# Kernel optimization log

Hardware: AMD Instinct MI355X
Metric: run time of the kernel (lower is better)

## Reference

```python
import jax, jax.numpy as jnp
import numpy as np

N_EMBED = 1024
HEAD_SIZE = 128
B, T = 4, 4096

def setup_inputs() -> dict:
    key = jax.random.key(0)
    kx, kk, kq, kv = jax.random.split(key, 4)
    s = (1.0 / np.sqrt(N_EMBED)).astype(np.float32)
    return {
        "x": jax.random.normal(kx, (B, T, N_EMBED), dtype=jnp.float32),
        "W_key": jax.random.normal(kk, (N_EMBED, HEAD_SIZE), dtype=jnp.float32) * s,
        "W_query": jax.random.normal(kq, (N_EMBED, HEAD_SIZE), dtype=jnp.float32) * s,
        "W_value": jax.random.normal(kv, (N_EMBED, HEAD_SIZE), dtype=jnp.float32) * s,
    }

def reference(x, W_key, W_query, W_value):
    # x: [B,T,C]; single-head causal attention. NOTE: scale is C**-0.5 (n_embed),
    # matching the original source (not head_size**-0.5).
    Bn, Tn, C = x.shape
    k = jnp.einsum('btc,cd->btd', x, W_key)    # [B,T,d]
    q = jnp.einsum('btc,cd->btd', x, W_query)  # [B,T,d]
    v = jnp.einsum('btc,cd->btd', x, W_value)  # [B,T,d]
    scores = jnp.einsum('btd,bsd->bts', q, k) * (C ** -0.5)  # [B,T,T]
    causal = jnp.tril(jnp.ones((Tn, Tn), dtype=bool))
    scores = jnp.where(causal[None, :, :], scores, -jnp.inf)
    attn = jax.nn.softmax(scores, axis=-1)
    return jnp.einsum('bts,bsd->btd', attn, v)
```

## Files before the change

### kernel.cpp

```cpp
#include <hip/hip_runtime.h>
#include <hip/hip_bf16.h>

typedef __attribute__((ext_vector_type(8))) short bf16x8;
typedef __attribute__((ext_vector_type(4))) float f32x4;
typedef __attribute__((ext_vector_type(4))) unsigned short us4;

__device__ __forceinline__ unsigned short f2bf(float f) {
    union { float f; unsigned u; } c; c.f = f;
    unsigned u = c.u;
    u += 0x7fffu + ((u >> 16) & 1u);
    return (unsigned short)(u >> 16);
}
__device__ __forceinline__ float bf2f(unsigned short h) {
    union { unsigned u; float f; } c; c.u = ((unsigned)h) << 16;
    return c.f;
}
__device__ __forceinline__ unsigned cvt_pk_bf16(float lo, float hi) {
    unsigned r;
    asm volatile("v_cvt_pk_bf16_f32 %0, %1, %2" : "=v"(r) : "v"(lo), "v"(hi));
    return r;
}
__device__ __forceinline__ void gload_lds16(const void* g, void* l) {
    __builtin_amdgcn_global_load_lds(
        (const __attribute__((address_space(1))) unsigned int*)g,
        (__attribute__((address_space(3))) unsigned int*)l, 16, 0, 0);
}

#define QSCALE 0.04508422f

__global__ __launch_bounds__(256) void wconv_kernel(
        const float* __restrict__ Wk, const float* __restrict__ Wq,
        const float* __restrict__ Wv, unsigned short* __restrict__ WbT) {
    int idx = blockIdx.x * 256 + threadIdx.x;
    int n = idx >> 10, kk = idx & 1023;
    const float* W = (n < 128) ? Wk : (n < 256) ? Wq : Wv;
    int col = n & 127;
    WbT[idx] = f2bf(W[kk * 128 + col]);
}

__global__ __launch_bounds__(512) void qkv_gemm_kernel(
        const float* __restrict__ x, const unsigned short* __restrict__ WbT,
        unsigned short* __restrict__ kw, unsigned short* __restrict__ qw,
        unsigned short* __restrict__ vTw) {
    __shared__ __align__(16) unsigned short Bl[2][192 * 64];
    __shared__ __align__(16) unsigned short Al[2][64 * 72];
    const int tid = threadIdx.x;
    const int m0 = (blockIdx.x >> 1) * 64;
    const int nb = blockIdx.x & 1;
    const int w = tid >> 6, l = tid & 63;
    const int l15 = l & 15, lh = l >> 4;
    const int wm = w >> 2, wn = w & 3;

    f32x4 acc[2][3] = {};

    const int srcsw = ((((l & 7) * 16) ^ ((l >> 3) << 4)) >> 1);
    const unsigned short* gB[3];
    #pragma unroll
    for (int it = 0; it < 3; ++it)
        gB[it] = WbT + (size_t)(nb * 192 + it * 64 + w * 8 + (l >> 3)) * 1024 + srcsw;

    const float* xr = &x[(size_t)(m0 + (tid >> 3)) * 1024 + (tid & 7) * 8];
    const int aoff = (tid >> 3) * 72 + (tid & 7) * 8;

    float4 aE0, aE1, aO0, aO1;

    #define STAGE_B(buf, t_) do { \
        _Pragma("unroll") \
        for (int it = 0; it < 3; ++it) \
            gload_lds16(gB[it] + (t_) * 64, &Bl[buf][(it * 64 + w * 8) * 64]); \
    } while (0)
    #define ISSUE_A(d0, d1, t_) do { \
        d0 = *(const float4*)(xr + (t_) * 64); \
        d1 = *(const float4*)(xr + (t_) * 64 + 4); } while (0)
    #define WRITE_A(buf, s0, s1) do { \
        uint4 pk_; \
        pk_.x = cvt_pk_bf16(s0.x, s0.y); pk_.y = cvt_pk_bf16(s0.z, s0.w); \
        pk_.z = cvt_pk_bf16(s1.x, s1.y); pk_.w = cvt_pk_bf16(s1.z, s1.w); \
        *(uint4*)&Al[buf][aoff] = pk_; } while (0)
    #define MFMA_ON(buf) do { \
        for (int kc = 0; kc < 2; ++kc) { \
            bf16x8 a_[2], bb_[3]; \
            for (int mi = 0; mi < 2; ++mi) \
                a_[mi] = *(const bf16x8*)&Al[buf][(wm * 32 + mi * 16 + l15) * 72 + kc * 32 + lh * 8]; \
            for (int ni = 0; ni < 3; ++ni) { \
                int n_ = wn * 48 + ni * 16 + l15; \
                bb_[ni] = *(const bf16x8*)((const char*)Bl[buf] + n_ * 128 + \
                        ((kc * 64 + lh * 16) ^ ((n_ & 7) << 4))); \
            } \
            for (int mi = 0; mi < 2; ++mi) \
                for (int ni = 0; ni < 3; ++ni) \
                    acc[mi][ni] = __builtin_amdgcn_mfma_f32_16x16x32_bf16( \
                            a_[mi], bb_[ni], acc[mi][ni], 0, 0, 0); \
        } } while (0)
    #define BAR(n_) do { \
        asm volatile("s_waitcnt vmcnt(" #n_ ") lgkmcnt(0)" ::: "memory"); \
        __builtin_amdgcn_sched_barrier(0); \
        __builtin_amdgcn_s_barrier(); } while (0)

    STAGE_B(0, 0);
    ISSUE_A(aE0, aE1, 0);
    ISSUE_A(aO0, aO1, 1);
    WRITE_A(0, aE0, aE1);
    BAR(2);

    #pragma unroll 1
    for (int tt = 0; tt < 8; ++tt) {
        const int t0 = tt * 2;
        STAGE_B(1, t0 + 1);
        if (t0 + 2 < 16) ISSUE_A(aE0, aE1, t0 + 2);
        MFMA_ON(0);
        WRITE_A(1, aO0, aO1);
        if (t0 + 2 < 16) BAR(2); else BAR(0);
        if (t0 + 2 < 16) {
            STAGE_B(0, t0 + 2);
            if (t0 + 3 < 16) ISSUE_A(aO0, aO1, t0 + 3);
            MFMA_ON(1);
            WRITE_A(0, aE0, aE1);
            if (t0 + 3 < 16) BAR(2); else BAR(0);
        } else {
            MFMA_ON(1);
        }
    }
    #undef STAGE_B
    #undef ISSUE_A
    #undef WRITE_A
    #undef MFMA_ON
    #undef BAR

    for (int mi = 0; mi < 2; ++mi)
        for (int ni = 0; ni < 3; ++ni) {
            int col = nb * 192 + wn * 48 + ni * 16 + l15;
            int sect = col >> 7, cc = col & 127;
            if (sect < 2) {
                unsigned short* dst = (sect == 0) ? kw : qw;
                float fs = (sect == 0) ? 1.0f : QSCALE;
                for (int i = 0; i < 4; ++i) {
                    int row = m0 + wm * 32 + mi * 16 + lh * 4 + i;
                    dst[(size_t)row * 128 + cc] = f2bf(acc[mi][ni][i] * fs);
                }
            } else {
                int trow0 = m0 + wm * 32 + mi * 16 + lh * 4;
                int b = trow0 >> 12, t0_ = trow0 & 4095;
                union { unsigned short u[4]; us4 v; } pk;
                for (int i = 0; i < 4; ++i) pk.u[i] = f2bf(acc[mi][ni][i]);
                *(us4*)&vTw[((size_t)(b * 128 + cc)) * 4096 + t0_] = pk.v;
            }
        }
}

__global__ __launch_bounds__(512) void attn_kernel(
        const unsigned short* __restrict__ kw, const unsigned short* __restrict__ qw,
        const unsigned short* __restrict__ vTw,
        unsigned short* __restrict__ pO, float* __restrict__ pL,
        int nCPB, int G, int TPC) {
    __shared__ __align__(16) unsigned short Kl[2][64 * 128];
    __shared__ __align__(16) unsigned short Vl[2][128 * 64];
    __shared__ __align__(16) unsigned short Pl[8][1024];

    const int tid = threadIdx.x;
    const int wgid = blockIdx.x;
    const int xcd = wgid & 7, slot = wgid >> 3;
    const int b = xcd >> 1, half = xcd & 1;
    const int cid = (nCPB - 1) - (slot * 2 + half);
    const int halfG = G >> 1;
    int a = 0;
    while (halfG * (a + 1) * (a + 2) <= cid) ++a;
    int rem = cid - halfG * a * (a + 1);
    const int g = G * a + rem / (a + 1);
    const int c = rem % (a + 1);
    const int kt0 = c * TPC;
    const int kt1 = min(kt0 + TPC, 2 * g + 2);

    const int w = tid >> 6, l = tid & 63;
    const int l15 = l & 15, lh = l >> 4;
    const int qrow0 = g * 128 + w * 16;

    bf16x8 qa[4];
    {
        size_t grow = (size_t)b * 4096 + qrow0 + l15;
        for (int cc = 0; cc < 4; ++cc)
            qa[cc] = *(const bf16x8*)&qw[grow * 128 + cc * 32 + lh * 8];
    }
    bf16x8 ones;
    for (int u = 0; u < 8; ++u) ones[u] = (short)0x3F80;

    f32x4 o[8] = {};
    f32x4 lsa = {0.f, 0.f, 0.f, 0.f};

    const int kc0 = 2 * w, kc1 = 2 * w + 1;
    const int kr0 = 4 * kc0 + (l >> 4), kr1 = 4 * kc1 + (l >> 4);
    const unsigned short* gk0 = kw + ((size_t)(b * 4096 + kr0)) * 128 +
            (((((l & 15) * 16) ^ ((kr0 & 7) << 4))) >> 1);
    const unsigned short* gk1 = kw + ((size_t)(b * 4096 + kr1)) * 128 +
            (((((l & 15) * 16) ^ ((kr1 & 7) << 4))) >> 1);
    const int vd0 = 8 * kc0 + (l >> 3), vd1 = 8 * kc1 + (l >> 3);
    const unsigned short* gv0 = vTw + ((size_t)(b * 128 + vd0)) * 4096 +
            (((((l & 7) * 16) ^ ((vd0 & 7) << 4))) >> 1);
    const unsigned short* gv1 = vTw + ((size_t)(b * 128 + vd1)) * 4096 +
            (((((l & 7) * 16) ^ ((vd1 & 7) << 4))) >> 1);

    #define STAGE(B_, kt_) do { \
        int kv_ = (kt_) * 64; \
        gload_lds16(gk0 + (size_t)kv_ * 128, &Kl[B_][kc0 * 512]); \
        gload_lds16(gk1 + (size_t)kv_ * 128, &Kl[B_][kc1 * 512]); \
        gload_lds16(gv0 + kv_, &Vl[B_][kc0 * 512]); \
        gload_lds16(gv1 + kv_, &Vl[B_][kc1 * 512]); } while (0)

    char* Plw = (char*)&Pl[w][0];

    STAGE(0, kt0);
    __syncthreads();
    int cur = 0;
    for (int kt = kt0; kt < kt1; ++kt) {
        if (kt + 1 < kt1) STAGE(cur ^ 1, kt + 1);
        const int kv0 = kt * 64;
        if (kv0 <= qrow0 + 15) {
            const char* Kc = (const char*)Kl[cur];
            const char* Vc = (const char*)Vl[cur];
            f32x4 s[4];
            __builtin_amdgcn_s_setprio(1);
            for (int ni = 0; ni < 4; ++ni) {
                s[ni] = (f32x4){0.f, 0.f, 0.f, 0.f};
                int kr = ni * 16 + l15;
                int sw = (kr & 7) << 4;
                for (int cc = 0; cc < 4; ++cc) {
                    bf16x8 bk = *(bf16x8*)(Kc + kr * 256 + ((lh * 16 + cc * 64) ^ sw));
                    s[ni] = __builtin_amdgcn_mfma_f32_16x16x32_bf16(bk, qa[cc], s[ni], 0, 0, 0);
                }
            }
            __builtin_amdgcn_s_setprio(0);

            if (kv0 + 63 > qrow0) {
                int qg = qrow0 + l15;
                for (int ni = 0; ni < 4; ++ni)
                    for (int i = 0; i < 4; ++i)
                        if (kv0 + ni * 16 + lh * 4 + i > qg) s[ni][i] = -INFINITY;
            }
            for (int ni = 0; ni < 4; ++ni) {
                float p0 = exp2f(s[ni][0]), p1 = exp2f(s[ni][1]);
                float p2 = exp2f(s[ni][2]), p3 = exp2f(s[ni][3]);
                uint2 pk;
                pk.x = cvt_pk_bf16(p0, p1);
                pk.y = cvt_pk_bf16(p2, p3);
                *(uint2*)(Plw + l15 * 128 + ((ni * 32 + lh * 8) ^ ((l15 & 7) << 4))) = pk;
            }
            bf16x8 pa[2];
            for (int kc = 0; kc < 2; ++kc)
                pa[kc] = *(bf16x8*)(Plw + l15 * 128 +
                        ((kc * 64 + lh * 16) ^ ((l15 & 7) << 4)));
            __builtin_amdgcn_s_setprio(1);
            lsa = __builtin_amdgcn_mfma_f32_16x16x32_bf16(pa[1], ones,
                  __builtin_amdgcn_mfma_f32_16x16x32_bf16(pa[0], ones, lsa, 0, 0, 0), 0, 0, 0);
            for (int nd = 0; nd < 8; ++nd) {
                int dr = nd * 16 + l15;
                int sw = (dr & 7) << 4;
                for (int kc = 0; kc < 2; ++kc) {
                    bf16x8 bv = *(bf16x8*)(Vc + dr * 128 + ((lh * 16 + kc * 64) ^ sw));
                    o[nd] = __builtin_amdgcn_mfma_f32_16x16x32_bf16(pa[kc], bv, o[nd], 0, 0, 0);
                }
            }
            __builtin_amdgcn_s_setprio(0);
        }
        __syncthreads();
        cur ^= 1;
    }
    #undef STAGE

    const int slot_ = b * nCPB + cid;
    unsigned short* po = pO + (size_t)slot_ * 16384;
    for (int nd = 0; nd < 8; ++nd)
        for (int i = 0; i < 4; ++i)
            po[(w * 16 + lh * 4 + i) * 128 + nd * 16 + l15] = f2bf(o[nd][i]);
    if (l15 == 0) {
        float* pl = pL + (size_t)slot_ * 128;
        for (int i = 0; i < 4; ++i)
            pl[w * 16 + lh * 4 + i] = lsa[i];
    }
}

__global__ __launch_bounds__(256) void combine_kernel(
        const unsigned short* __restrict__ pO, const float* __restrict__ pL,
        float* __restrict__ out, int nCPB, int G) {
    int idx = blockIdx.x * 256 + threadIdx.x;
    int row = idx >> 4, d8 = (idx & 15) * 8;
    int b = row >> 12, t = row & 4095;
    int g = t >> 7, rowin = t & 127;
    int a = g / G;
    int nch = a + 1;
    int base = b * nCPB + (G >> 1) * a * (a + 1) + (g - G * a) * (a + 1);

    float den = 0.f;
    float num[8] = {0.f, 0.f, 0.f, 0.f, 0.f, 0.f, 0.f, 0.f};
    for (int cc = 0; cc < nch; ++cc) {
        den += pL[(size_t)(base + cc) * 128 + rowin];
        bf16x8 ov = *(const bf16x8*)&pO[(size_t)(base + cc) * 16384 + rowin * 128 + d8];
        for (int u = 0; u < 8; ++u)
            num[u] += bf2f((unsigned short)ov[u]);
    }
    float inv = 1.f / den;
    for (int u = 0; u < 8; ++u)
        out[(size_t)row * 128 + d8 + u] = num[u] * inv;
}

extern "C" void kernel_launch(void* const* d_in, const int* in_sizes, int n_in,
                              void* d_out, int out_size, void* d_ws, size_t ws_size,
                              hipStream_t stream) {
    const float* x  = (const float*)d_in[0];
    const float* Wk = (const float*)d_in[1];
    const float* Wq = (const float*)d_in[2];
    const float* Wv = (const float*)d_in[3];
    float* out = (float*)d_out;

    char* ws = (char*)d_ws;
    unsigned short* WbT = (unsigned short*)(ws);
    unsigned short* kw  = (unsigned short*)(ws + 786432);
    unsigned short* qw  = (unsigned short*)(ws + 786432 + 4194304);
    unsigned short* vTw = (unsigned short*)(ws + 786432 + 2 * 4194304);
    size_t base = 786432 + 3 * (size_t)4194304;

    int nCPB, G, TPC;
    size_t need4 = base + (size_t)1088 * 32768 + (size_t)1088 * 512;
    if (ws_size >= need4) { nCPB = 272; G = 2; TPC = 4; }
    else                  { nCPB = 144; G = 4; TPC = 8; }
    int nslots = 4 * nCPB;
    unsigned short* pO = (unsigned short*)(ws + base);
    float*          pL = (float*)(ws + base + (size_t)nslots * 32768);

    wconv_kernel<<<1536, 256, 0, stream>>>(Wk, Wq, Wv, WbT);
    qkv_gemm_kernel<<<512, 512, 0, stream>>>(x, WbT, kw, qw, vTw);
    attn_kernel<<<nslots, 512, 0, stream>>>(kw, qw, vTw, pO, pL, nCPB, G, TPC);
    combine_kernel<<<1024, 256, 0, stream>>>(pO, pL, out, nCPB, G);
}
```

Before: 81.79 us.

## Double query rows per warp and stage K/V through registers

Each warp now handles 32 query rows (two 16-row MFMA tiles) instead of 16, so every K and V fragment read from LDS feeds twice as many MFMAs. The work split becomes fixed 256-row query groups with 4-tile KV chunks, giving 544 workgroups and half the partial slots for the combine step. The async global-to-LDS double buffer is replaced by a register prefetch with a single LDS buffer and two barriers per tile. This raises register pressure and drops the workspace-size fallback path.

```diff
diff --git a/kernel.cpp b/kernel.cpp
--- a/kernel.cpp
+++ b/kernel.cpp
@@ -151,149 +151,158 @@
 __global__ __launch_bounds__(512) void attn_kernel(
         const unsigned short* __restrict__ kw, const unsigned short* __restrict__ qw,
         const unsigned short* __restrict__ vTw,
-        unsigned short* __restrict__ pO, float* __restrict__ pL,
-        int nCPB, int G, int TPC) {
-    __shared__ __align__(16) unsigned short Kl[2][64 * 128];
-    __shared__ __align__(16) unsigned short Vl[2][128 * 64];
-    __shared__ __align__(16) unsigned short Pl[8][1024];
+        unsigned short* __restrict__ pO, float* __restrict__ pL) {
+    __shared__ __align__(16) unsigned short Kl[64 * 128];
+    __shared__ __align__(16) unsigned short Vl[128 * 64];
+    __shared__ __align__(16) unsigned short Pl[8][2048];
 
     const int tid = threadIdx.x;
     const int wgid = blockIdx.x;
     const int xcd = wgid & 7, slot = wgid >> 3;
-    const int b = xcd >> 1, half = xcd & 1;
-    const int cid = (nCPB - 1) - (slot * 2 + half);
-    const int halfG = G >> 1;
-    int a = 0;
-    while (halfG * (a + 1) * (a + 2) <= cid) ++a;
-    int rem = cid - halfG * a * (a + 1);
-    const int g = G * a + rem / (a + 1);
-    const int c = rem % (a + 1);
-    const int kt0 = c * TPC;
-    const int kt1 = min(kt0 + TPC, 2 * g + 2);
+    const int b = xcd >> 1;
+    const int cid = (xcd & 1) * 68 + slot;
+    int g = 0;
+    while ((g + 1) * (g + 2) / 2 <= cid) ++g;
+    const int c = cid - g * (g + 1) / 2;
+    const int kt0 = c * 4, kt1 = kt0 + 4;
 
     const int w = tid >> 6, l = tid & 63;
     const int l15 = l & 15, lh = l >> 4;
-    const int qrow0 = g * 128 + w * 16;
-
-    bf16x8 qa[4];
+    const int qrow0 = g * 256 + w * 32;
+
+    bf16x8 qa0[4], qa1[4];
     {
-        size_t grow = (size_t)b * 4096 + qrow0 + l15;
-        for (int cc = 0; cc < 4; ++cc)
-            qa[cc] = *(const bf16x8*)&qw[grow * 128 + cc * 32 + lh * 8];
+        size_t gr0 = (size_t)b * 4096 + qrow0 + l15;
+        size_t gr1 = gr0 + 16;
+        for (int cc = 0; cc < 4; ++cc) {
+            qa0[cc] = *(const bf16x8*)&qw[gr0 * 128 + cc * 32 + lh * 8];
+            qa1[cc] = *(const bf16x8*)&qw[gr1 * 128 + cc * 32 + lh * 8];
+        }
     }
     bf16x8 ones;
     for (int u = 0; u < 8; ++u) ones[u] = (short)0x3F80;
 
-    f32x4 o[8] = {};
-    f32x4 lsa = {0.f, 0.f, 0.f, 0.f};
-
-    const int kc0 = 2 * w, kc1 = 2 * w + 1;
-    const int kr0 = 4 * kc0 + (l >> 4), kr1 = 4 * kc1 + (l >> 4);
-    const unsigned short* gk0 = kw + ((size_t)(b * 4096 + kr0)) * 128 +
-            (((((l & 15) * 16) ^ ((kr0 & 7) << 4))) >> 1);
-    const unsigned short* gk1 = kw + ((size_t)(b * 4096 + kr1)) * 128 +
-            (((((l & 15) * 16) ^ ((kr1 & 7) << 4))) >> 1);
-    const int vd0 = 8 * kc0 + (l >> 3), vd1 = 8 * kc1 + (l >> 3);
-    const unsigned short* gv0 = vTw + ((size_t)(b * 128 + vd0)) * 4096 +
-            (((((l & 7) * 16) ^ ((vd0 & 7) << 4))) >> 1);
-    const unsigned short* gv1 = vTw + ((size_t)(b * 128 + vd1)) * 4096 +
-            (((((l & 7) * 16) ^ ((vd1 & 7) << 4))) >> 1);
-
-    #define STAGE(B_, kt_) do { \
-        int kv_ = (kt_) * 64; \
-        gload_lds16(gk0 + (size_t)kv_ * 128, &Kl[B_][kc0 * 512]); \
-        gload_lds16(gk1 + (size_t)kv_ * 128, &Kl[B_][kc1 * 512]); \
-        gload_lds16(gv0 + kv_, &Vl[B_][kc0 * 512]); \
-        gload_lds16(gv1 + kv_, &Vl[B_][kc1 * 512]); } while (0)
+    f32x4 o0[8] = {}, o1[8] = {};
+    f32x4 lsa0 = {0.f, 0.f, 0.f, 0.f}, lsa1 = {0.f, 0.f, 0.f, 0.f};
+
+    const int kr_ = tid >> 3;
+    const int vd_ = tid >> 2;
+    bf16x8 kReg[2], vReg[2];
+    auto issue = [&](int kt) {
+        int kv0 = kt * 64;
+        const unsigned short* ks = &kw[((size_t)(b * 4096 + kv0 + kr_)) * 128 + (tid & 7) * 16];
+        kReg[0] = *(const bf16x8*)ks;
+        kReg[1] = *(const bf16x8*)(ks + 8);
+        const unsigned short* vs = &vTw[((size_t)(b * 128 + vd_)) * 4096 + kv0 + (tid & 3) * 16];
+        vReg[0] = *(const bf16x8*)vs;
+        vReg[1] = *(const bf16x8*)(vs + 8);
+    };
 
     char* Plw = (char*)&Pl[w][0];
 
-    STAGE(0, kt0);
-    __syncthreads();
-    int cur = 0;
+    issue(kt0);
     for (int kt = kt0; kt < kt1; ++kt) {
-        if (kt + 1 < kt1) STAGE(cur ^ 1, kt + 1);
+        __syncthreads();
+        for (int it = 0; it < 2; ++it)
+            *(bf16x8*)((char*)Kl + kr_ * 256 +
+                    (((tid & 7) * 32 + it * 16) ^ ((kr_ & 7) << 4))) = kReg[it];
+        for (int it = 0; it < 2; ++it)
+            *(bf16x8*)((char*)Vl + vd_ * 128 +
+                    (((tid & 3) * 32 + it * 16) ^ ((vd_ & 7) << 4))) = vReg[it];
+        __syncthreads();
+        if (kt + 1 < kt1) issue(kt + 1);
+
         const int kv0 = kt * 64;
-        if (kv0 <= qrow0 + 15) {
-            const char* Kc = (const char*)Kl[cur];
-            const char* Vc = (const char*)Vl[cur];
-            f32x4 s[4];
-            __builtin_amdgcn_s_setprio(1);
-            for (int ni = 0; ni < 4; ++ni) {
-                s[ni] = (f32x4){0.f, 0.f, 0.f, 0.f};
-                int kr = ni * 16 + l15;
-                int sw = (kr & 7) << 4;
-                for (int cc = 0; cc < 4; ++cc) {
-                    bf16x8 bk = *(bf16x8*)(Kc + kr * 256 + ((lh * 16 + cc * 64) ^ sw));
-                    s[ni] = __builtin_amdgcn_mfma_f32_16x16x32_bf16(bk, qa[cc], s[ni], 0, 0, 0);
+        if (kv0 > qrow0 + 31) continue;
+
+        f32x4 s0[4], s1[4];
+        __builtin_amdgcn_s_setprio(1);
+        for (int ni = 0; ni < 4; ++ni) {
+            s0[ni] = (f32x4){0.f, 0.f, 0.f, 0.f};
+            s1[ni] = (f32x4){0.f, 0.f, 0.f, 0.f};
+            int kr = ni * 16 + l15;
+            int sw = (kr & 7) << 4;
+            for (int cc = 0; cc < 4; ++cc) {
+                bf16x8 bk = *(bf16x8*)((char*)Kl + kr * 256 + ((lh * 16 + cc * 64) ^ sw));
+                s0[ni] = __builtin_amdgcn_mfma_f32_16x16x32_bf16(bk, qa0[cc], s0[ni], 0, 0, 0);
+                s1[ni] = __builtin_amdgcn_mfma_f32_16x16x32_bf16(bk, qa1[cc], s1[ni], 0, 0, 0);
+            }
+        }
+        __builtin_amdgcn_s_setprio(0);
+
+        if (kv0 + 63 > qrow0) {
+            int q0 = qrow0 + l15, q1 = q0 + 16;
+            for (int ni = 0; ni < 4; ++ni)
+                for (int i = 0; i < 4; ++i) {
+                    int kvp = kv0 + ni * 16 + lh * 4 + i;
+                    if (kvp > q0) s0[ni][i] = -INFINITY;
+                    if (kvp > q1) s1[ni][i] = -INFINITY;
                 }
+        }
+        for (int ni = 0; ni < 4; ++ni) {
+            uint2 pk;
+            pk.x = cvt_pk_bf16(exp2f(s0[ni][0]), exp2f(s0[ni][1]));
+            pk.y = cvt_pk_bf16(exp2f(s0[ni][2]), exp2f(s0[ni][3]));
+            *(uint2*)(Plw + l15 * 128 + ((ni * 32 + lh * 8) ^ ((l15 & 7) << 4))) = pk;
+            pk.x = cvt_pk_bf16(exp2f(s1[ni][0]), exp2f(s1[ni][1]));
+            pk.y = cvt_pk_bf16(exp2f(s1[ni][2]), exp2f(s1[ni][3]));
+            *(uint2*)(Plw + (16 + l15) * 128 + ((ni * 32 + lh * 8) ^ ((l15 & 7) << 4))) = pk;
+        }
+        bf16x8 pa0[2], pa1[2];
+        for (int kc = 0; kc < 2; ++kc) {
+            pa0[kc] = *(bf16x8*)(Plw + l15 * 128 +
+                    ((kc * 64 + lh * 16) ^ ((l15 & 7) << 4)));
+            pa1[kc] = *(bf16x8*)(Plw + (16 + l15) * 128 +
+                    ((kc * 64 + lh * 16) ^ ((l15 & 7) << 4)));
+        }
+        __builtin_amdgcn_s_setprio(1);
+        lsa0 = __builtin_amdgcn_mfma_f32_16x16x32_bf16(pa0[1], ones,
+               __builtin_amdgcn_mfma_f32_16x16x32_bf16(pa0[0], ones, lsa0, 0, 0, 0), 0, 0, 0);
+        lsa1 = __builtin_amdgcn_mfma_f32_16x16x32_bf16(pa1[1], ones,
+               __builtin_amdgcn_mfma_f32_16x16x32_bf16(pa1[0], ones, lsa1, 0, 0, 0), 0, 0, 0);
+        for (int nd = 0; nd < 8; ++nd) {
+            int dr = nd * 16 + l15;
+            int sw = (dr & 7) << 4;
+            for (int kc = 0; kc < 2; ++kc) {
+                bf16x8 bv = *(bf16x8*)((char*)Vl + dr * 128 + ((lh * 16 + kc * 64) ^ sw));
+                o0[nd] = __builtin_amdgcn_mfma_f32_16x16x32_bf16(pa0[kc], bv, o0[nd], 0, 0, 0);
+                o1[nd] = __builtin_amdgcn_mfma_f32_16x16x32_bf16(pa1[kc], bv, o1[nd], 0, 0, 0);
             }
-            __builtin_amdgcn_s_setprio(0);
-
-            if (kv0 + 63 > qrow0) {
-                int qg = qrow0 + l15;
-                for (int ni = 0; ni < 4; ++ni)
-                    for (int i = 0; i < 4; ++i)
-                        if (kv0 + ni * 16 + lh * 4 + i > qg) s[ni][i] = -INFINITY;
-            }
-            for (int ni = 0; ni < 4; ++ni) {
-                float p0 = exp2f(s[ni][0]), p1 = exp2f(s[ni][1]);
-                float p2 = exp2f(s[ni][2]), p3 = exp2f(s[ni][3]);
-                uint2 pk;
-                pk.x = cvt_pk_bf16(p0, p1);
-                pk.y = cvt_pk_bf16(p2, p3);
-                *(uint2*)(Plw + l15 * 128 + ((ni * 32 + lh * 8) ^ ((l15 & 7) << 4))) = pk;
-            }
-            bf16x8 pa[2];
-            for (int kc = 0; kc < 2; ++kc)
-                pa[kc] = *(bf16x8*)(Plw + l15 * 128 +
-                        ((kc * 64 + lh * 16) ^ ((l15 & 7) << 4)));
-            __builtin_amdgcn_s_setprio(1);
-            lsa = __builtin_amdgcn_mfma_f32_16x16x32_bf16(pa[1], ones,
-                  __builtin_amdgcn_mfma_f32_16x16x32_bf16(pa[0], ones, lsa, 0, 0, 0), 0, 0, 0);
-            for (int nd = 0; nd < 8; ++nd) {
-                int dr = nd * 16 + l15;
-                int sw = (dr & 7) << 4;
-                for (int kc = 0; kc < 2; ++kc) {
-                    bf16x8 bv = *(bf16x8*)(Vc + dr * 128 + ((lh * 16 + kc * 64) ^ sw));
-                    o[nd] = __builtin_amdgcn_mfma_f32_16x16x32_bf16(pa[kc], bv, o[nd], 0, 0, 0);
-                }
-            }
-            __builtin_amdgcn_s_setprio(0);
-        }
-        __syncthreads();
-        cur ^= 1;
-    }
-    #undef STAGE
-
-    const int slot_ = b * nCPB + cid;
-    unsigned short* po = pO + (size_t)slot_ * 16384;
+        }
+        __builtin_amdgcn_s_setprio(0);
+    }
+
+    const int slot_ = b * 136 + cid;
+    unsigned short* po = pO + (size_t)slot_ * 32768;
     for (int nd = 0; nd < 8; ++nd)
-        for (int i = 0; i < 4; ++i)
-            po[(w * 16 + lh * 4 + i) * 128 + nd * 16 + l15] = f2bf(o[nd][i]);
+        for (int i = 0; i < 4; ++i) {
+            po[(w * 32 + lh * 4 + i) * 128 + nd * 16 + l15]      = f2bf(o0[nd][i]);
+            po[(w * 32 + 16 + lh * 4 + i) * 128 + nd * 16 + l15] = f2bf(o1[nd][i]);
+        }
     if (l15 == 0) {
-        float* pl = pL + (size_t)slot_ * 128;
-        for (int i = 0; i < 4; ++i)
-            pl[w * 16 + lh * 4 + i] = lsa[i];
+        float* pl = pL + (size_t)slot_ * 256;
+        for (int i = 0; i < 4; ++i) {
+            pl[w * 32 + lh * 4 + i]      = lsa0[i];
+            pl[w * 32 + 16 + lh * 4 + i] = lsa1[i];
+        }
     }
 }
 
 __global__ __launch_bounds__(256) void combine_kernel(
         const unsigned short* __restrict__ pO, const float* __restrict__ pL,
-        float* __restrict__ out, int nCPB, int G) {
+        float* __restrict__ out) {
     int idx = blockIdx.x * 256 + threadIdx.x;
     int row = idx >> 4, d8 = (idx & 15) * 8;
     int b = row >> 12, t = row & 4095;
-    int g = t >> 7, rowin = t & 127;
-    int a = g / G;
-    int nch = a + 1;
-    int base = b * nCPB + (G >> 1) * a * (a + 1) + (g - G * a) * (a + 1);
+    int g = t >> 8, rowin = t & 255;
+    int nch = g + 1;
+    int base = b * 136 + g * (g + 1) / 2;
 
     float den = 0.f;
     float num[8] = {0.f, 0.f, 0.f, 0.f, 0.f, 0.f, 0.f, 0.f};
     for (int cc = 0; cc < nch; ++cc) {
-        den += pL[(size_t)(base + cc) * 128 + rowin];
-        bf16x8 ov = *(const bf16x8*)&pO[(size_t)(base + cc) * 16384 + rowin * 128 + d8];
+        den += pL[(size_t)(base + cc) * 256 + rowin];
+        bf16x8 ov = *(const bf16x8*)&pO[(size_t)(base + cc) * 32768 + rowin * 128 + d8];
         for (int u = 0; u < 8; ++u)
             num[u] += bf2f((unsigned short)ov[u]);
     }
@@ -317,17 +326,11 @@
     unsigned short* qw  = (unsigned short*)(ws + 786432 + 4194304);
     unsigned short* vTw = (unsigned short*)(ws + 786432 + 2 * 4194304);
     size_t base = 786432 + 3 * (size_t)4194304;
-
-    int nCPB, G, TPC;
-    size_t need4 = base + (size_t)1088 * 32768 + (size_t)1088 * 512;
-    if (ws_size >= need4) { nCPB = 272; G = 2; TPC = 4; }
-    else                  { nCPB = 144; G = 4; TPC = 8; }
-    int nslots = 4 * nCPB;
     unsigned short* pO = (unsigned short*)(ws + base);
-    float*          pL = (float*)(ws + base + (size_t)nslots * 32768);
+    float*          pL = (float*)(ws + base + (size_t)544 * 65536);
 
     wconv_kernel<<<1536, 256, 0, stream>>>(Wk, Wq, Wv, WbT);
     qkv_gemm_kernel<<<512, 512, 0, stream>>>(x, WbT, kw, qw, vTw);
-    attn_kernel<<<nslots, 512, 0, stream>>>(kw, qw, vTw, pO, pL, nCPB, G, TPC);
-    combine_kernel<<<1024, 256, 0, stream>>>(pO, pL, out, nCPB, G);
-}
+    attn_kernel<<<544, 512, 0, stream>>>(kw, qw, vTw, pO, pL);
+    combine_kernel<<<1024, 256, 0, stream>>>(pO, pL, out);
+}
```

After: 87.40 us. 1.07x slower.

## Stage K/V tiles through registers into single-buffered LDS instead of async global_load_lds

Applied to the files above, without the earlier changes.

Replaces the double-buffered direct global-to-LDS async loads with register prefetch. Each thread loads the next K/V tile into registers, then writes it into a single swizzled LDS buffer between two barriers. This halves LDS use for K/V and adds a waves_per_eu hint, aiming for more resident workgroups per CU. In exchange it adds an extra barrier per iteration, register pressure from the prefetch, and VGPR-to-LDS write traffic.

```diff
diff --git a/kernel.cpp b/kernel.cpp
--- a/kernel.cpp
+++ b/kernel.cpp
@@ -148,13 +148,15 @@
         }
 }
 
-__global__ __launch_bounds__(512) void attn_kernel(
+__global__ __launch_bounds__(512)
+__attribute__((amdgpu_waves_per_eu(2, 4)))
+void attn_kernel(
         const unsigned short* __restrict__ kw, const unsigned short* __restrict__ qw,
         const unsigned short* __restrict__ vTw,
         unsigned short* __restrict__ pO, float* __restrict__ pL,
         int nCPB, int G, int TPC) {
-    __shared__ __align__(16) unsigned short Kl[2][64 * 128];
-    __shared__ __align__(16) unsigned short Vl[2][128 * 64];
+    __shared__ __align__(16) unsigned short Kl[64 * 128];
+    __shared__ __align__(16) unsigned short Vl[128 * 64];
     __shared__ __align__(16) unsigned short Pl[8][1024];
 
     const int tid = threadIdx.x;
@@ -187,84 +189,80 @@
     f32x4 o[8] = {};
     f32x4 lsa = {0.f, 0.f, 0.f, 0.f};
 
-    const int kc0 = 2 * w, kc1 = 2 * w + 1;
-    const int kr0 = 4 * kc0 + (l >> 4), kr1 = 4 * kc1 + (l >> 4);
-    const unsigned short* gk0 = kw + ((size_t)(b * 4096 + kr0)) * 128 +
-            (((((l & 15) * 16) ^ ((kr0 & 7) << 4))) >> 1);
-    const unsigned short* gk1 = kw + ((size_t)(b * 4096 + kr1)) * 128 +
-            (((((l & 15) * 16) ^ ((kr1 & 7) << 4))) >> 1);
-    const int vd0 = 8 * kc0 + (l >> 3), vd1 = 8 * kc1 + (l >> 3);
-    const unsigned short* gv0 = vTw + ((size_t)(b * 128 + vd0)) * 4096 +
-            (((((l & 7) * 16) ^ ((vd0 & 7) << 4))) >> 1);
-    const unsigned short* gv1 = vTw + ((size_t)(b * 128 + vd1)) * 4096 +
-            (((((l & 7) * 16) ^ ((vd1 & 7) << 4))) >> 1);
-
-    #define STAGE(B_, kt_) do { \
-        int kv_ = (kt_) * 64; \
-        gload_lds16(gk0 + (size_t)kv_ * 128, &Kl[B_][kc0 * 512]); \
-        gload_lds16(gk1 + (size_t)kv_ * 128, &Kl[B_][kc1 * 512]); \
-        gload_lds16(gv0 + kv_, &Vl[B_][kc0 * 512]); \
-        gload_lds16(gv1 + kv_, &Vl[B_][kc1 * 512]); } while (0)
+    const int kr_ = tid >> 3;
+    const int vd_ = tid >> 2;
+    bf16x8 kReg[2], vReg[2];
+    auto issue = [&](int kt) {
+        int kv0 = kt * 64;
+        const unsigned short* ks = &kw[((size_t)(b * 4096 + kv0 + kr_)) * 128 + (tid & 7) * 16];
+        kReg[0] = *(const bf16x8*)ks;
+        kReg[1] = *(const bf16x8*)(ks + 8);
+        const unsigned short* vs = &vTw[((size_t)(b * 128 + vd_)) * 4096 + kv0 + (tid & 3) * 16];
+        vReg[0] = *(const bf16x8*)vs;
+        vReg[1] = *(const bf16x8*)(vs + 8);
+    };
 
     char* Plw = (char*)&Pl[w][0];
 
-    STAGE(0, kt0);
-    __syncthreads();
-    int cur = 0;
+    issue(kt0);
     for (int kt = kt0; kt < kt1; ++kt) {
-        if (kt + 1 < kt1) STAGE(cur ^ 1, kt + 1);
+        __syncthreads();
+        for (int it = 0; it < 2; ++it)
+            *(bf16x8*)((char*)Kl + kr_ * 256 +
+                    (((tid & 7) * 32 + it * 16) ^ ((kr_ & 7) << 4))) = kReg[it];
+        for (int it = 0; it < 2; ++it)
+            *(bf16x8*)((char*)Vl + vd_ * 128 +
+                    (((tid & 3) * 32 + it * 16) ^ ((vd_ & 7) << 4))) = vReg[it];
+        __syncthreads();
+        if (kt + 1 < kt1) issue(kt + 1);
+
         const int kv0 = kt * 64;
-        if (kv0 <= qrow0 + 15) {
-            const char* Kc = (const char*)Kl[cur];
-            const char* Vc = (const char*)Vl[cur];
-            f32x4 s[4];
-            __builtin_amdgcn_s_setprio(1);
-            for (int ni = 0; ni < 4; ++ni) {
-                s[ni] = (f32x4){0.f, 0.f, 0.f, 0.f};
-                int kr = ni * 16 + l15;
-                int sw = (kr & 7) << 4;
-                for (int cc = 0; cc < 4; ++cc) {
-                    bf16x8 bk = *(bf16x8*)(Kc + kr * 256 + ((lh * 16 + cc * 64) ^ sw));
-                    s[ni] = __builtin_amdgcn_mfma_f32_16x16x32_bf16(bk, qa[cc], s[ni], 0, 0, 0);
-                }
+        if (kv0 > qrow0 + 15) continue;
+
+        f32x4 s[4];
+        __builtin_amdgcn_s_setprio(1);
+        for (int ni = 0; ni < 4; ++ni) {
+            s[ni] = (f32x4){0.f, 0.f, 0.f, 0.f};
+            int kr = ni * 16 + l15;
+            int sw = (kr & 7) << 4;
+            for (int cc = 0; cc < 4; ++cc) {
+                bf16x8 bk = *(bf16x8*)((char*)Kl + kr * 256 + ((lh * 16 + cc * 64) ^ sw));
+                s[ni] = __builtin_amdgcn_mfma_f32_16x16x32_bf16(bk, qa[cc], s[ni], 0, 0, 0);
             }
-            __builtin_amdgcn_s_setprio(0);
-
-            if (kv0 + 63 > qrow0) {
-                int qg = qrow0 + l15;
-                for (int ni = 0; ni < 4; ++ni)
-                    for (int i = 0; i < 4; ++i)
-                        if (kv0 + ni * 16 + lh * 4 + i > qg) s[ni][i] = -INFINITY;
+        }
+        __builtin_amdgcn_s_setprio(0);
+
+        if (kv0 + 63 > qrow0) {
+            int qg = qrow0 + l15;
+            for (int ni = 0; ni < 4; ++ni)
+                for (int i = 0; i < 4; ++i)
+                    if (kv0 + ni * 16 + lh * 4 + i > qg) s[ni][i] = -INFINITY;
+        }
+        for (int ni = 0; ni < 4; ++ni) {
+            float p0 = exp2f(s[ni][0]), p1 = exp2f(s[ni][1]);
+            float p2 = exp2f(s[ni][2]), p3 = exp2f(s[ni][3]);
+            uint2 pk;
+            pk.x = cvt_pk_bf16(p0, p1);
+            pk.y = cvt_pk_bf16(p2, p3);
+            *(uint2*)(Plw + l15 * 128 + ((ni * 32 + lh * 8) ^ ((l15 & 7) << 4))) = pk;
+        }
+        bf16x8 pa[2];
+        for (int kc = 0; kc < 2; ++kc)
+            pa[kc] = *(bf16x8*)(Plw + l15 * 128 +
+                    ((kc * 64 + lh * 16) ^ ((l15 & 7) << 4)));
+        __builtin_amdgcn_s_setprio(1);
+        lsa = __builtin_amdgcn_mfma_f32_16x16x32_bf16(pa[1], ones,
+              __builtin_amdgcn_mfma_f32_16x16x32_bf16(pa[0], ones, lsa, 0, 0, 0), 0, 0, 0);
+        for (int nd = 0; nd < 8; ++nd) {
+            int dr = nd * 16 + l15;
+            int sw = (dr & 7) << 4;
+            for (int kc = 0; kc < 2; ++kc) {
+                bf16x8 bv = *(bf16x8*)((char*)Vl + dr * 128 + ((lh * 16 + kc * 64) ^ sw));
+                o[nd] = __builtin_amdgcn_mfma_f32_16x16x32_bf16(pa[kc], bv, o[nd], 0, 0, 0);
             }
-            for (int ni = 0; ni < 4; ++ni) {
-                float p0 = exp2f(s[ni][0]), p1 = exp2f(s[ni][1]);
-                float p2 = exp2f(s[ni][2]), p3 = exp2f(s[ni][3]);
-                uint2 pk;
-                pk.x = cvt_pk_bf16(p0, p1);
-                pk.y = cvt_pk_bf16(p2, p3);
-                *(uint2*)(Plw + l15 * 128 + ((ni * 32 + lh * 8) ^ ((l15 & 7) << 4))) = pk;
-            }
-            bf16x8 pa[2];
-            for (int kc = 0; kc < 2; ++kc)
-                pa[kc] = *(bf16x8*)(Plw + l15 * 128 +
-                        ((kc * 64 + lh * 16) ^ ((l15 & 7) << 4)));
-            __builtin_amdgcn_s_setprio(1);
-            lsa = __builtin_amdgcn_mfma_f32_16x16x32_bf16(pa[1], ones,
-                  __builtin_amdgcn_mfma_f32_16x16x32_bf16(pa[0], ones, lsa, 0, 0, 0), 0, 0, 0);
-            for (int nd = 0; nd < 8; ++nd) {
-                int dr = nd * 16 + l15;
-                int sw = (dr & 7) << 4;
-                for (int kc = 0; kc < 2; ++kc) {
-                    bf16x8 bv = *(bf16x8*)(Vc + dr * 128 + ((lh * 16 + kc * 64) ^ sw));
-                    o[nd] = __builtin_amdgcn_mfma_f32_16x16x32_bf16(pa[kc], bv, o[nd], 0, 0, 0);
-                }
-            }
-            __builtin_amdgcn_s_setprio(0);
-        }
-        __syncthreads();
-        cur ^= 1;
-    }
-    #undef STAGE
+        }
+        __builtin_amdgcn_s_setprio(0);
+    }
 
     const int slot_ = b * nCPB + cid;
     unsigned short* po = pO + (size_t)slot_ * 16384;
```

Result: no change. 80.61 us (-1.4%).
